# Kernel tuning notes

Hardware: AMD Instinct MI355X
Metric: run time of the kernel (lower is better)

## Reference

```python
import jax, jax.numpy as jnp
import numpy as np

N_NODES = 100000
BN_EPS = 1e-5


def gcn_conv(x, row, col, ew, W, b, n):
    # PyG GCNConv (normalize=True, add_self_loops=True):
    # add self loops with weight 1, symmetric deg^-1/2 normalization,
    # message = norm * (x @ W)[row], scatter-add at col (target), + bias.
    h = x @ W  # [N, F_out]
    loop = jnp.arange(n)
    row_f = jnp.concatenate([row, loop])
    col_f = jnp.concatenate([col, loop])
    ew_f = jnp.concatenate([ew, jnp.ones((n,), dtype=ew.dtype)])
    deg = jax.ops.segment_sum(ew_f, col_f, num_segments=n)  # [N]
    dis = jnp.where(deg > 0, jax.lax.rsqrt(jnp.maximum(deg, 1e-30)), 0.0)
    norm = dis[row_f] * ew_f * dis[col_f]  # [E+N]
    msg = norm[:, None] * h[row_f]  # [E+N, F_out]
    agg = jax.ops.segment_sum(msg, col_f, num_segments=n)
    return agg + b


def batchnorm(h, gamma, beta):
    mean = h.mean(axis=0)
    var = h.var(axis=0)  # biased, as torch BN training-mode normalization
    return gamma * (h - mean) * jax.lax.rsqrt(var + BN_EPS) + beta


def setup_inputs() -> dict:
    key = jax.random.key(0)
    ks = jax.random.split(key, 12)
    N, E, D = N_NODES, 3200000, 256
    x = jax.random.normal(ks[0], (N, D), dtype=jnp.float32)
    edge_index = jax.random.randint(ks[1], (2, E), 0, N, dtype=jnp.int64)
    edge_weight = jax.random.uniform(ks[2], (E,), dtype=jnp.float32)
    s = 1.0 / np.sqrt(D)
    W1 = jax.random.uniform(ks[3], (D, D), jnp.float32, -s, s)
    b1 = jnp.zeros((D,), jnp.float32)
    g1 = jnp.ones((D,), jnp.float32)
    be1 = jnp.zeros((D,), jnp.float32)
    W2 = jax.random.uniform(ks[4], (D, D), jnp.float32, -s, s)
    b2 = jnp.zeros((D,), jnp.float32)
    g2 = jnp.ones((D,), jnp.float32)
    be2 = jnp.zeros((D,), jnp.float32)
    return {"x": x, "edge_index": edge_index, "edge_weight": edge_weight,
            "W1": W1, "b1": b1, "g1": g1, "be1": be1,
            "W2": W2, "b2": b2, "g2": g2, "be2": be2}


def reference(x, edge_index, edge_weight, W1, b1, g1, be1, W2, b2, g2, be2):
    n = x.shape[0]
    row, col = edge_index[0], edge_index[1]
    h = gcn_conv(x, row, col, edge_weight, W1, b1, n)
    h = jax.nn.relu(batchnorm(h, g1, be1))
    h = gcn_conv(h, row, col, edge_weight, W2, b2, n)
    h = batchnorm(h, g2, be2)
    # in_dim == out_dim -> proj is Identity
    return jax.nn.relu(h + x)
```

## Files before the change

### kernel.cpp

```cpp
#include <hip/hip_runtime.h>
#include <hip/hip_bf16.h>

#define D 256
#define BN_EPS 1e-5f
#define CHUNK 4096
#define NPB 512
#define CAP_B 20480

typedef __attribute__((ext_vector_type(8))) short bf16x8;
typedef __attribute__((ext_vector_type(4))) float f32x4;
typedef unsigned long long ull;
typedef unsigned char uchar;

__device__ inline uint pack2_rne(float a, float b) {
    uint ua = __builtin_bit_cast(uint, a);
    ua = ua + 0x7FFFu + ((ua >> 16) & 1u);
    uint ub = __builtin_bit_cast(uint, b);
    ub = ub + 0x7FFFu + ((ub >> 16) & 1u);
    return (ua >> 16) | (ub & 0xFFFF0000u);
}
__device__ inline ushort f2bf_rne(float a) {
    uint ua = __builtin_bit_cast(uint, a);
    ua = ua + 0x7FFFu + ((ua >> 16) & 1u);
    return (ushort)(ua >> 16);
}
__device__ inline float bf2f(ushort u) {
    uint x = ((uint)u) << 16;
    return __builtin_bit_cast(float, x);
}
__device__ inline uint pack_edge(uint rowbits, uint ewbits) {
    uint b15 = (ewbits + 0x8000u) >> 16;
    return (rowbits & 0x1FFFFu) | (b15 << 17);
}
__device__ inline float edge_ew(uint e) {
    return __builtin_bit_cast(float, (e >> 17) << 16);
}

__global__ __launch_bounds__(256) void init_fast_kernel(int* __restrict__ cursor,
                                                        float* __restrict__ stats) {
    int t = threadIdx.x;
    cursor[t] = t * CAP_B;
    stats[t] = 0.f;
    stats[t + 256] = 0.f;
    stats[t + 512] = 0.f;
    stats[t + 768] = 0.f;
}

__global__ __launch_bounds__(256) void bin_kernel(const int* __restrict__ row,
                                                  const int* __restrict__ col,
                                                  const float* __restrict__ ew,
                                                  int* __restrict__ cursor,
                                                  uint2* __restrict__ bdata, int E) {
    __shared__ int h[256];
    __shared__ int base[256];
    int t = threadIdx.x;
    h[t] = 0;
    __syncthreads();
    int cb = blockIdx.x * CHUNK;
    int cols[CHUNK / 256];
#pragma unroll
    for (int i = 0; i < CHUNK / 256; ++i) {
        int e = cb + i * 256 + t;
        int c = (e < E) ? col[e] : -1;
        cols[i] = c;
        if (c >= 0) atomicAdd(&h[c >> 9], 1);
    }
    __syncthreads();
    if (h[t]) base[t] = atomicAdd(&cursor[t], h[t]);
    __syncthreads();
    h[t] = 0;
    __syncthreads();
#pragma unroll
    for (int i = 0; i < CHUNK / 256; ++i) {
        int e = cb + i * 256 + t;
        int c = cols[i];
        if (c >= 0) {
            int b = c >> 9;
            int pos = base[b] + atomicAdd(&h[b], 1);
            if (pos < (b + 1) * CAP_B) {
                uint xv = (uint)row[e] | ((uint)(c & (NPB - 1)) << 17);
                bdata[pos] = make_uint2(xv, __float_as_uint(ew[e]));
            }
        }
    }
}

__global__ __launch_bounds__(256) void final_csr_kernel(const uint2* __restrict__ bdata,
                                                        const int* __restrict__ cursor,
                                                        uint* __restrict__ csr,
                                                        int* __restrict__ offs,
                                                        int* __restrict__ cnts,
                                                        float2* __restrict__ dscale, int N) {
    __shared__ int cnt[NPB];
    __shared__ float deg[NPB];
    __shared__ int sp[256];
    int bkt = blockIdx.x;
    int t = threadIdx.x;
    int beg = bkt * CAP_B;
    int end = min(cursor[bkt], beg + CAP_B);
    cnt[t] = 0; cnt[t + 256] = 0;
    deg[t] = 0.f; deg[t + 256] = 0.f;
    __syncthreads();
    for (int i = beg + t; i < end; i += 256) {
        uint2 v = bdata[i];
        int cl = v.x >> 17;
        atomicAdd(&cnt[cl], 1);
        atomicAdd(&deg[cl], __uint_as_float(v.y));
    }
    __syncthreads();
    int a0 = cnt[2 * t], a1 = cnt[2 * t + 1];
    sp[t] = a0 + a1;
    __syncthreads();
    for (int o = 1; o < 256; o <<= 1) {
        int add = (t >= o) ? sp[t - o] : 0;
        __syncthreads();
        sp[t] += add;
        __syncthreads();
    }
    int ex = sp[t] - (a0 + a1);
    int n0 = bkt * NPB + 2 * t;
    if (n0 < N) {
        offs[n0] = beg + ex;
        cnts[n0] = a0;
        dscale[n0].x = rsqrtf(deg[2 * t] + 1.0f);
    }
    if (n0 + 1 < N) {
        offs[n0 + 1] = beg + ex + a0;
        cnts[n0 + 1] = a1;
        dscale[n0 + 1].x = rsqrtf(deg[2 * t + 1] + 1.0f);
    }
    __syncthreads();
    cnt[2 * t] = ex;
    cnt[2 * t + 1] = ex + a0;
    __syncthreads();
    for (int i = beg + t; i < end; i += 256) {
        uint2 v = bdata[i];
        int cl = v.x >> 17;
        int pos = beg + atomicAdd(&cnt[cl], 1);
        csr[pos] = pack_edge(v.x, v.y);
    }
}

__global__ __launch_bounds__(256) void count_deg_kernel(const int* __restrict__ col,
                                                        const float* __restrict__ ew,
                                                        ull* __restrict__ dg, int E) {
    int e = blockIdx.x * 256 + threadIdx.x;
    if (e < E) {
        int c = col[e];
        uint q = (uint)(ew[e] * 8388608.0f + 0.5f);
        atomicAdd(&dg[c], (1ull << 40) | (ull)q);
    }
}

__global__ __launch_bounds__(256) void dis_cnt_kernel(const ull* __restrict__ dg,
                                                      float2* __restrict__ dscale,
                                                      int* __restrict__ cnt,
                                                      int* __restrict__ cnts,
                                                      float* __restrict__ stats, int N) {
    int i = blockIdx.x * 256 + threadIdx.x;
    if (i < 1024) stats[i] = 0.0f;
    if (i < N) {
        ull g = dg[i];
        int c = (int)(g >> 40);
        cnt[i] = c;
        cnts[i] = c;
        float deg = (float)(g & ((1ull << 40) - 1)) * (1.0f / 8388608.0f);
        dscale[i].x = rsqrtf(deg + 1.0f);
    }
}

__global__ __launch_bounds__(256) void scan_reduce(const int* __restrict__ cnt,
                                                   int* __restrict__ bsum, int N) {
    __shared__ int sd[256];
    int t = threadIdx.x;
    int i = blockIdx.x * 256 + t;
    sd[t] = (i < N) ? cnt[i] : 0;
    __syncthreads();
    for (int o = 128; o > 0; o >>= 1) {
        if (t < o) sd[t] += sd[t + o];
        __syncthreads();
    }
    if (t == 0) bsum[blockIdx.x] = sd[0];
}

__global__ __launch_bounds__(512) void scan_bsum(int* __restrict__ bsum, int B) {
    __shared__ int sd[512];
    int t = threadIdx.x;
    int v = (t < B) ? bsum[t] : 0;
    sd[t] = v;
    __syncthreads();
    for (int o = 1; o < 512; o <<= 1) {
        int add = (t >= o) ? sd[t - o] : 0;
        __syncthreads();
        sd[t] += add;
        __syncthreads();
    }
    if (t < B) bsum[t] = sd[t] - v;
}

__global__ __launch_bounds__(256) void scan_final(const int* __restrict__ cnt,
                                                  const int* __restrict__ bsum,
                                                  int* __restrict__ offs,
                                                  int* __restrict__ next, int N, int E) {
    __shared__ int sd[256];
    int t = threadIdx.x;
    int i = blockIdx.x * 256 + t;
    int v = (i < N) ? cnt[i] : 0;
    sd[t] = v;
    __syncthreads();
    for (int o = 1; o < 256; o <<= 1) {
        int add = (t >= o) ? sd[t - o] : 0;
        __syncthreads();
        sd[t] += add;
        __syncthreads();
    }
    int excl = sd[t] - v + bsum[blockIdx.x];
    if (i < N) {
        offs[i] = excl;
        next[i] = excl;
    }
    if (i == 0 && blockIdx.x == 0) offs[N] = E;
}

__global__ __launch_bounds__(256) void fill_kernel(const int* __restrict__ row,
                                                   const int* __restrict__ col,
                                                   const float* __restrict__ ew,
                                                   int* __restrict__ next,
                                                   uint* __restrict__ csr, int E) {
    int e = blockIdx.x * 256 + threadIdx.x;
    if (e < E) {
        int pos = atomicAdd(&next[col[e]], 1);
        csr[pos] = pack_edge((uint)row[e], __float_as_uint(ew[e]));
    }
}

__global__ __launch_bounds__(256) void prep_wt2_kernel(const float* __restrict__ W1,
                                                       const float* __restrict__ W2,
                                                       ushort* __restrict__ Wt1,
                                                       ushort* __restrict__ Wt2) {
    __shared__ float tile[64][65];
    const float* W = blockIdx.y ? W2 : W1;
    ushort* Wt = blockIdx.y ? Wt2 : Wt1;
    int t = threadIdx.x;
    int k0 = (blockIdx.x >> 2) * 64;
    int n0 = (blockIdx.x & 3) * 64;
#pragma unroll
    for (int it = 0; it < 16; ++it) {
        int idx = it * 256 + t;
        int r = idx >> 6, c = idx & 63;
        tile[r][c] = W[(size_t)(k0 + r) * D + n0 + c];
    }
    __syncthreads();
#pragma unroll
    for (int it = 0; it < 16; ++it) {
        int idx = it * 256 + t;
        int n = idx >> 6, k = idx & 63;
        Wt[(size_t)(n0 + n) * D + k0 + k] = f2bf_rne(tile[k][n]);
    }
}

template <int MODE>
__global__ __launch_bounds__(256) void gemm_mfma(const float* __restrict__ Xf,
                                                 const ushort* __restrict__ Xb,
                                                 const float* __restrict__ stats,
                                                 const float* __restrict__ gamma,
                                                 const float* __restrict__ beta,
                                                 const ushort* __restrict__ Wt,
                                                 uchar* __restrict__ Hq,
                                                 float2* __restrict__ dscale,
                                                 int N, float invN) {
    __shared__ char wt_lds[32 * 1024];
    __shared__ float cf_lds[2][MODE ? 256 : 1];
    const int t = threadIdx.x;
    const int wv = t >> 6;
    const int l = t & 63;
    const int ln = l & 15;
    const int kg0 = l >> 4;
    const int rblk = blockIdx.x * 128 + wv * 32;

    if constexpr (MODE == 1) {
        float mean = stats[t] * invN;
        float var = fmaxf(stats[D + t] * invN - mean * mean, 0.0f);
        float sc = gamma[t] * rsqrtf(var + BN_EPS);
        cf_lds[0][t] = sc;
        cf_lds[1][t] = beta[t] - sc * mean;
    }

    f32x4 acc[2][16];
#pragma unroll
    for (int g = 0; g < 2; ++g)
#pragma unroll
        for (int i = 0; i < 16; ++i) acc[g][i] = f32x4{0.f, 0.f, 0.f, 0.f};

    const int sg_n = t >> 3;
    const int sg_g = t & 7;
    const int sg_lds = (sg_g ^ (sg_n & 7)) * 16;

    for (int kt = 0; kt < 4; ++kt) {
        const int k0 = kt * 64;
        __syncthreads();
#pragma unroll
        for (int p = 0; p < 8; ++p) {
            int n = p * 32 + sg_n;
            uint4 v = *reinterpret_cast<const uint4*>(Wt + (size_t)n * 256 + k0 + sg_g * 8);
            *reinterpret_cast<uint4*>(&wt_lds[n * 128 + sg_lds]) = v;
        }
        __syncthreads();
#pragma unroll
        for (int kh = 0; kh < 2; ++kh) {
            const int kb = k0 + kh * 32 + kg0 * 8;
            bf16x8 afr[2];
#pragma unroll
            for (int g = 0; g < 2; ++g) {
                int arow = rblk + g * 16 + ln;
                afr[g] = bf16x8{};
                if (arow < N) {
                    if constexpr (MODE == 0) {
                        const float* ap = Xf + (size_t)arow * D + kb;
                        float4 f0 = *reinterpret_cast<const float4*>(ap);
                        float4 f1 = *reinterpret_cast<const float4*>(ap + 4);
                        uint4 u;
                        u.x = (__builtin_bit_cast(uint, f0.x) >> 16) | (__builtin_bit_cast(uint, f0.y) & 0xFFFF0000u);
                        u.y = (__builtin_bit_cast(uint, f0.z) >> 16) | (__builtin_bit_cast(uint, f0.w) & 0xFFFF0000u);
                        u.z = (__builtin_bit_cast(uint, f1.x) >> 16) | (__builtin_bit_cast(uint, f1.y) & 0xFFFF0000u);
                        u.w = (__builtin_bit_cast(uint, f1.z) >> 16) | (__builtin_bit_cast(uint, f1.w) & 0xFFFF0000u);
                        afr[g] = __builtin_bit_cast(bf16x8, u);
                    } else {
                        bf16x8 raw = *reinterpret_cast<const bf16x8*>(Xb + (size_t)arow * D + kb);
                        f32x4 scA = *reinterpret_cast<const f32x4*>(&cf_lds[0][kb]);
                        f32x4 scB = *reinterpret_cast<const f32x4*>(&cf_lds[0][kb + 4]);
                        f32x4 shA = *reinterpret_cast<const f32x4*>(&cf_lds[1][kb]);
                        f32x4 shB = *reinterpret_cast<const f32x4*>(&cf_lds[1][kb + 4]);
                        uint4 u;
                        u.x = pack2_rne(fmaxf(scA[0] * bf2f((ushort)raw[0]) + shA[0], 0.f),
                                        fmaxf(scA[1] * bf2f((ushort)raw[1]) + shA[1], 0.f));
                        u.y = pack2_rne(fmaxf(scA[2] * bf2f((ushort)raw[2]) + shA[2], 0.f),
                                        fmaxf(scA[3] * bf2f((ushort)raw[3]) + shA[3], 0.f));
                        u.z = pack2_rne(fmaxf(scB[0] * bf2f((ushort)raw[4]) + shB[0], 0.f),
                                        fmaxf(scB[1] * bf2f((ushort)raw[5]) + shB[1], 0.f));
                        u.w = pack2_rne(fmaxf(scB[2] * bf2f((ushort)raw[6]) + shB[2], 0.f),
                                        fmaxf(scB[3] * bf2f((ushort)raw[7]) + shB[3], 0.f));
                        afr[g] = __builtin_bit_cast(bf16x8, u);
                    }
                }
            }
            const int s = ln * 128 + (((kg0 + kh * 4) ^ (ln & 7)) * 16);
            const char* bbase = &wt_lds[s];
#pragma unroll
            for (int ct = 0; ct < 16; ++ct) {
                bf16x8 bfr = *reinterpret_cast<const bf16x8*>(bbase + ct * 2048);
                acc[0][ct] = __builtin_amdgcn_mfma_f32_16x16x32_bf16(afr[0], bfr, acc[0][ct], 0, 0, 0);
                acc[1][ct] = __builtin_amdgcn_mfma_f32_16x16x32_bf16(afr[1], bfr, acc[1][ct], 0, 0, 0);
            }
        }
    }

    __syncthreads();
    uchar* qtile = (uchar*)wt_lds;
#pragma unroll
    for (int g = 0; g < 2; ++g) {
#pragma unroll
        for (int r = 0; r < 4; ++r) {
            float am = 0.f;
#pragma unroll
            for (int ct = 0; ct < 16; ++ct) am = fmaxf(am, fabsf(acc[g][ct][r]));
#pragma unroll
            for (int mk = 1; mk < 16; mk <<= 1) am = fmaxf(am, __shfl_xor(am, mk));
            float qs = am > 0.f ? 127.0f / am : 0.f;
            int rloc = wv * 32 + g * 16 + kg0 * 4 + r;
            int rowi = blockIdx.x * 128 + rloc;
            if (ln == 0 && rowi < N) dscale[rowi].y = am * (1.0f / 127.0f);
#pragma unroll
            for (int ct = 0; ct < 16; ++ct) {
                int q = (int)rintf(acc[g][ct][r] * qs) + 128;
                qtile[rloc * 256 + ct * 16 + ln] = (uchar)q;
            }
        }
    }
    __syncthreads();
    const uint4* qt4 = reinterpret_cast<const uint4*>(qtile);
#pragma unroll
    for (int k = 0; k < 8; ++k) {
        int j = k * 256 + t;
        int rowi = blockIdx.x * 128 + (j >> 4);
        if (rowi < N)
            *reinterpret_cast<uint4*>(Hq + (size_t)rowi * 256 + (j & 15) * 16) = qt4[j];
    }
}

__global__ __launch_bounds__(128) void gather_q_kernel(const uchar* __restrict__ hq,
                                                       ushort* __restrict__ ha,
                                                       const uint* __restrict__ csr,
                                                       const int* __restrict__ offs,
                                                       const int* __restrict__ cnts,
                                                       const float2* __restrict__ dscale,
                                                       int N) {
    int node = blockIdx.x;
    int t = threadIdx.x;
    int wv = t >> 6;
    int ln = t & 63;
    int beg = offs[node];
    int cnt = cnts[node];
    float2 dsn = dscale[node];
    float dc = dsn.x;

    float a0 = 0.f, a1 = 0.f, a2 = 0.f, a3 = 0.f, S = 0.f;
    if (wv == 0) {
        float ws = dc * dc * dsn.y;
        uint q0 = *reinterpret_cast<const uint*>(hq + (size_t)node * 256 + ln * 4);
        a0 = ws * (float)(q0 & 0xFF);
        a1 = ws * (float)((q0 >> 8) & 0xFF);
        a2 = ws * (float)((q0 >> 16) & 0xFF);
        a3 = ws * (float)(q0 >> 24);
        S = ws;
    }

    __shared__ int2 sc[128];

    for (int base = 0; base < cnt; base += 128) {
        int m = min(128, cnt - base);
        if (t < m) {
            uint v = __builtin_nontemporal_load(csr + beg + base + t);
            int r = (int)(v & 0x1FFFFu);
            float2 dsr = dscale[r];
            float w = edge_ew(v) * dsr.x * dc * dsr.y;
            sc[t] = make_int2(r, __float_as_int(w));
        }
        __syncthreads();
        int i = wv;
        for (; i + 16 <= m; i += 16) {
            float w[8];
            uint v[8];
#pragma unroll
            for (int j = 0; j < 8; ++j) {
                int2 e = sc[i + 2 * j];
                w[j] = __int_as_float(e.y);
                v[j] = *reinterpret_cast<const uint*>(hq + (size_t)e.x * 256 + ln * 4);
            }
#pragma unroll
            for (int j = 0; j < 8; ++j) {
                a0 = fmaf(w[j], (float)(v[j] & 0xFF), a0);
                a1 = fmaf(w[j], (float)((v[j] >> 8) & 0xFF), a1);
                a2 = fmaf(w[j], (float)((v[j] >> 16) & 0xFF), a2);
                a3 = fmaf(w[j], (float)(v[j] >> 24), a3);
                S += w[j];
            }
        }
        for (; i < m; i += 2) {
            int2 e = sc[i];
            float w = __int_as_float(e.y);
            uint v = *reinterpret_cast<const uint*>(hq + (size_t)e.x * 256 + ln * 4);
            a0 = fmaf(w, (float)(v & 0xFF), a0);
            a1 = fmaf(w, (float)((v >> 8) & 0xFF), a1);
            a2 = fmaf(w, (float)((v >> 16) & 0xFF), a2);
            a3 = fmaf(w, (float)(v >> 24), a3);
            S += w;
        }
        __syncthreads();
    }

    __shared__ float4 redA[64];
    __shared__ float redS[64];
    if (wv == 1) {
        redA[ln] = make_float4(a0, a1, a2, a3);
        redS[ln] = S;
    }
    __syncthreads();
    if (wv == 0) {
        float4 rb = redA[ln];
        float Sb = redS[ln];
        a0 += rb.x; a1 += rb.y; a2 += rb.z; a3 += rb.w;
        S += Sb;
        float f0 = a0 - 128.0f * S;
        float f1 = a1 - 128.0f * S;
        float f2 = a2 - 128.0f * S;
        float f3 = a3 - 128.0f * S;
        uint2 p;
        p.x = pack2_rne(f0, f1);
        p.y = pack2_rne(f2, f3);
        reinterpret_cast<uint2*>(ha + (size_t)node * D)[ln] = p;
    }
}

__global__ __launch_bounds__(256) void stats_bf16_kernel(const ushort* __restrict__ ha,
                                                         float* __restrict__ stats, int N) {
    __shared__ float ls[512];
    int t = threadIdx.x;
    int tq = t & 63;
    int tr = t >> 6;
    float s[4] = {0.f, 0.f, 0.f, 0.f};
    float q[4] = {0.f, 0.f, 0.f, 0.f};
    for (int i = blockIdx.x * 4 + tr; i < N; i += gridDim.x * 4) {
        uint2 u = *reinterpret_cast<const uint2*>(ha + (size_t)i * D + tq * 4);
        float v0 = bf2f((ushort)u.x), v1 = bf2f((ushort)(u.x >> 16));
        float v2 = bf2f((ushort)u.y), v3 = bf2f((ushort)(u.y >> 16));
        s[0] += v0; q[0] += v0 * v0;
        s[1] += v1; q[1] += v1 * v1;
        s[2] += v2; q[2] += v2 * v2;
        s[3] += v3; q[3] += v3 * v3;
    }
    ls[t] = 0.f; ls[t + 256] = 0.f;
    __syncthreads();
#pragma unroll
    for (int j = 0; j < 4; ++j) {
        int c = tq * 4 + j;
        atomicAdd(&ls[c], s[j]);
        atomicAdd(&ls[256 + c], q[j]);
    }
    __syncthreads();
    for (int i = t; i < 512; i += 256)
        unsafeAtomicAdd(&stats[i], ls[i]);
}

__global__ __launch_bounds__(256) void final_kernel(const ushort* __restrict__ ha,
                                                    const float* __restrict__ x,
                                                    const float* __restrict__ stats2,
                                                    const float* __restrict__ gamma,
                                                    const float* __restrict__ beta,
                                                    float* __restrict__ out,
                                                    int N, float invN) {
    __shared__ float cf[2][256];
    int t = threadIdx.x;
    {
        float mean = stats2[t] * invN;
        float var = fmaxf(stats2[D + t] * invN - mean * mean, 0.0f);
        float sc = gamma[t] * rsqrtf(var + BN_EPS);
        cf[0][t] = sc;
        cf[1][t] = beta[t] - sc * mean;
    }
    __syncthreads();
    size_t i = (size_t)blockIdx.x * 256 + t;
    size_t total = (size_t)N * (D / 4);
    if (i >= total) return;
    int c0 = (int)((i * 4) & (D - 1));
    uint2 h = reinterpret_cast<const uint2*>(ha)[i];
    f32x4 xv = *(reinterpret_cast<const f32x4*>(x) + i);
    f32x4 sc4 = *reinterpret_cast<const f32x4*>(&cf[0][c0]);
    f32x4 sh4 = *reinterpret_cast<const f32x4*>(&cf[1][c0]);
    f32x4 o;
    o[0] = fmaxf(sc4[0] * bf2f((ushort)h.x) + sh4[0] + xv[0], 0.0f);
    o[1] = fmaxf(sc4[1] * bf2f((ushort)(h.x >> 16)) + sh4[1] + xv[1], 0.0f);
    o[2] = fmaxf(sc4[2] * bf2f((ushort)h.y) + sh4[2] + xv[2], 0.0f);
    o[3] = fmaxf(sc4[3] * bf2f((ushort)(h.y >> 16)) + sh4[3] + xv[3], 0.0f);
    __builtin_nontemporal_store(o, reinterpret_cast<f32x4*>(out) + i);
}

extern "C" void kernel_launch(void* const* d_in, const int* in_sizes, int n_in,
                              void* d_out, int out_size, void* d_ws, size_t ws_size,
                              hipStream_t stream) {
    const float* x  = (const float*)d_in[0];
    const int* eidx = (const int*)d_in[1];
    const float* ew = (const float*)d_in[2];
    const float* W1 = (const float*)d_in[3];
    const float* g1  = (const float*)d_in[5];
    const float* be1 = (const float*)d_in[6];
    const float* W2  = (const float*)d_in[7];
    const float* g2  = (const float*)d_in[9];
    const float* be2 = (const float*)d_in[10];
    float* out = (float*)d_out;

    const int N = in_sizes[0] / D;
    const int E = in_sizes[2];
    const int* row = eidx;
    const int* col = eidx + E;
    const float invN = 1.0f / (float)N;

    uchar* hq    = (uchar*)d_ws;
    ushort* ha   = (ushort*)(hq + (size_t)N * 256);
    ushort* Wt1  = ha + (size_t)N * D;
    ushort* Wt2  = Wt1 + 65536;
    float* stats = (float*)(Wt2 + 65536);
    float2* dscale = (float2*)(stats + 1024);
    int*   offs  = (int*)(dscale + N);
    int*   cnts  = offs + (N + 1);

    size_t head = (size_t)N * 256 + (size_t)N * D * 2 + (size_t)65536 * 4 + 1024 * 4
                + (size_t)N * 8 + (size_t)(N + 1) * 4 + (size_t)N * 4;

    const int nb = (N + NPB - 1) / NPB;
    const int nchunk = (E + CHUNK - 1) / CHUNK;
    const int scanB = (N + 255) / 256;
    const int gemmB = (N + 127) / 128;
    const int gElems4 = (N * (D / 4) + 255) / 256;

    size_t need_fast = head + 256 * 4 + 16 + (size_t)nb * CAP_B * 12;
    const bool fast = (N < (1 << 17)) && (nb <= 256) && (ws_size >= need_fast)
                   && ((size_t)nb * CAP_B >= (size_t)E);

    uint* csr;

    if (fast) {
        int* cursor = cnts + N;
        uintptr_t p = ((uintptr_t)(cursor + 256) + 15) & ~(uintptr_t)15;
        uint2* bdata = (uint2*)p;
        csr = (uint*)(bdata + (size_t)nb * CAP_B);

        init_fast_kernel<<<1, 256, 0, stream>>>(cursor, stats);
        bin_kernel<<<nchunk, 256, 0, stream>>>(row, col, ew, cursor, bdata, E);
        final_csr_kernel<<<nb, 256, 0, stream>>>(bdata, cursor, csr, offs, cnts, dscale, N);
    } else {
        int* cntnext = cnts + N;
        ull* dg   = (ull*)(cntnext + N);
        int* bsum = (int*)dg;
        csr = (uint*)(dg + N);
        hipMemsetAsync(dg, 0, (size_t)N * 8, stream);
        count_deg_kernel<<<(E + 255) / 256, 256, 0, stream>>>(col, ew, dg, E);
        dis_cnt_kernel<<<scanB, 256, 0, stream>>>(dg, dscale, cntnext, cnts, stats, N);
        scan_reduce<<<scanB, 256, 0, stream>>>(cntnext, bsum, N);
        scan_bsum<<<1, 512, 0, stream>>>(bsum, scanB);
        scan_final<<<scanB, 256, 0, stream>>>(cntnext, bsum, offs, cntnext, N, E);
        fill_kernel<<<(E + 255) / 256, 256, 0, stream>>>(row, col, ew, cntnext, csr, E);
    }

    prep_wt2_kernel<<<dim3(16, 2), 256, 0, stream>>>(W1, W2, Wt1, Wt2);

    gemm_mfma<0><<<gemmB, 256, 0, stream>>>(x, nullptr, nullptr, nullptr, nullptr,
                                            Wt1, hq, dscale, N, invN);
    gather_q_kernel<<<N, 128, 0, stream>>>(hq, ha, csr, offs, cnts, dscale, N);
    stats_bf16_kernel<<<1024, 256, 0, stream>>>(ha, stats, N);

    gemm_mfma<1><<<gemmB, 256, 0, stream>>>(nullptr, ha, stats, g1, be1,
                                            Wt2, hq, dscale, N, invN);
    gather_q_kernel<<<N, 128, 0, stream>>>(hq, ha, csr, offs, cnts, dscale, N);
    stats_bf16_kernel<<<1024, 256, 0, stream>>>(ha, stats + 512, N);

    final_kernel<<<gElems4, 256, 0, stream>>>(ha, x, stats + 512, g2, be2, out, N, invN);
}
```

Baseline: 627.5 us.

## Gather with one wavefront per node using 16-byte loads and shuffles

Measured after the change: 599.0 us. -4.5%, faster.

```diff
diff --git a/kernel.cpp b/kernel.cpp
--- a/kernel.cpp
+++ b/kernel.cpp
@@ -388,97 +388,79 @@
     }
 }
 
-__global__ __launch_bounds__(128) void gather_q_kernel(const uchar* __restrict__ hq,
+__global__ __launch_bounds__(256) void gather_q_kernel(const uchar* __restrict__ hq,
                                                        ushort* __restrict__ ha,
                                                        const uint* __restrict__ csr,
                                                        const int* __restrict__ offs,
                                                        const int* __restrict__ cnts,
                                                        const float2* __restrict__ dscale,
                                                        int N) {
-    int node = blockIdx.x;
-    int t = threadIdx.x;
-    int wv = t >> 6;
-    int ln = t & 63;
+    int wv = threadIdx.x >> 6;
+    int lane = threadIdx.x & 63;
+    int node = blockIdx.x * 4 + wv;
+    if (node >= N) return;
     int beg = offs[node];
     int cnt = cnts[node];
     float2 dsn = dscale[node];
     float dc = dsn.x;
-
-    float a0 = 0.f, a1 = 0.f, a2 = 0.f, a3 = 0.f, S = 0.f;
-    if (wv == 0) {
-        float ws = dc * dc * dsn.y;
-        uint q0 = *reinterpret_cast<const uint*>(hq + (size_t)node * 256 + ln * 4);
-        a0 = ws * (float)(q0 & 0xFF);
-        a1 = ws * (float)((q0 >> 8) & 0xFF);
-        a2 = ws * (float)((q0 >> 16) & 0xFF);
-        a3 = ws * (float)(q0 >> 24);
-        S = ws;
-    }
-
-    __shared__ int2 sc[128];
-
-    for (int base = 0; base < cnt; base += 128) {
-        int m = min(128, cnt - base);
-        if (t < m) {
-            uint v = __builtin_nontemporal_load(csr + beg + base + t);
-            int r = (int)(v & 0x1FFFFu);
+    int g = lane >> 4;
+    int u = lane & 15;
+
+    float acc[16];
+#pragma unroll
+    for (int j = 0; j < 16; ++j) acc[j] = 0.f;
+    float S = 0.f;
+
+    int total = cnt + 1;
+    for (int base = 0; base < total; base += 64) {
+        int m = min(64, total - base);
+        int gi = base + lane;
+        int r = node;
+        float w = 0.f;
+        if (gi < cnt) {
+            uint v = __builtin_nontemporal_load(csr + beg + gi);
+            r = (int)(v & 0x1FFFFu);
             float2 dsr = dscale[r];
-            float w = edge_ew(v) * dsr.x * dc * dsr.y;
-            sc[t] = make_int2(r, __float_as_int(w));
+            w = edge_ew(v) * dsr.x * dc * dsr.y;
+        } else if (gi == cnt) {
+            w = dc * dc * dsn.y;
         }
-        __syncthreads();
-        int i = wv;
-        for (; i + 16 <= m; i += 16) {
-            float w[8];
-            uint v[8];
-#pragma unroll
-            for (int j = 0; j < 8; ++j) {
-                int2 e = sc[i + 2 * j];
-                w[j] = __int_as_float(e.y);
-                v[j] = *reinterpret_cast<const uint*>(hq + (size_t)e.x * 256 + ln * 4);
-            }
-#pragma unroll
-            for (int j = 0; j < 8; ++j) {
-                a0 = fmaf(w[j], (float)(v[j] & 0xFF), a0);
-                a1 = fmaf(w[j], (float)((v[j] >> 8) & 0xFF), a1);
-                a2 = fmaf(w[j], (float)((v[j] >> 16) & 0xFF), a2);
-                a3 = fmaf(w[j], (float)(v[j] >> 24), a3);
-                S += w[j];
+        S += w;
+        for (int i = 0; i < m; i += 4) {
+            int src = i + g;
+            int er = __shfl(r, src);
+            float we = __shfl(w, src);
+            uint4 q = *reinterpret_cast<const uint4*>(hq + (size_t)er * 256 + u * 16);
+#pragma unroll
+            for (int b = 0; b < 4; ++b) {
+                uint qq = (&q.x)[b];
+                acc[b * 4 + 0] = fmaf(we, (float)(qq & 0xFF), acc[b * 4 + 0]);
+                acc[b * 4 + 1] = fmaf(we, (float)((qq >> 8) & 0xFF), acc[b * 4 + 1]);
+                acc[b * 4 + 2] = fmaf(we, (float)((qq >> 16) & 0xFF), acc[b * 4 + 2]);
+                acc[b * 4 + 3] = fmaf(we, (float)(qq >> 24), acc[b * 4 + 3]);
             }
         }
-        for (; i < m; i += 2) {
-            int2 e = sc[i];
-            float w = __int_as_float(e.y);
-            uint v = *reinterpret_cast<const uint*>(hq + (size_t)e.x * 256 + ln * 4);
-            a0 = fmaf(w, (float)(v & 0xFF), a0);
-            a1 = fmaf(w, (float)((v >> 8) & 0xFF), a1);
-            a2 = fmaf(w, (float)((v >> 16) & 0xFF), a2);
-            a3 = fmaf(w, (float)(v >> 24), a3);
-            S += w;
-        }
-        __syncthreads();
-    }
-
-    __shared__ float4 redA[64];
-    __shared__ float redS[64];
-    if (wv == 1) {
-        redA[ln] = make_float4(a0, a1, a2, a3);
-        redS[ln] = S;
-    }
-    __syncthreads();
-    if (wv == 0) {
-        float4 rb = redA[ln];
-        float Sb = redS[ln];
-        a0 += rb.x; a1 += rb.y; a2 += rb.z; a3 += rb.w;
-        S += Sb;
-        float f0 = a0 - 128.0f * S;
-        float f1 = a1 - 128.0f * S;
-        float f2 = a2 - 128.0f * S;
-        float f3 = a3 - 128.0f * S;
-        uint2 p;
-        p.x = pack2_rne(f0, f1);
-        p.y = pack2_rne(f2, f3);
-        reinterpret_cast<uint2*>(ha + (size_t)node * D)[ln] = p;
+    }
+
+#pragma unroll
+    for (int j = 0; j < 16; ++j) {
+        float a = acc[j];
+        a += __shfl_xor(a, 16);
+        a += __shfl_xor(a, 32);
+        acc[j] = a;
+    }
+#pragma unroll
+    for (int mk = 1; mk < 64; mk <<= 1) S += __shfl_xor(S, mk);
+
+    if (g == 0) {
+        float c = 128.0f * S;
+        uint o[8];
+#pragma unroll
+        for (int j = 0; j < 8; ++j)
+            o[j] = pack2_rne(acc[2 * j] - c, acc[2 * j + 1] - c);
+        uint4* dst = reinterpret_cast<uint4*>(ha + (size_t)node * D + u * 16);
+        dst[0] = make_uint4(o[0], o[1], o[2], o[3]);
+        dst[1] = make_uint4(o[4], o[5], o[6], o[7]);
     }
 }
 
@@ -614,14 +596,16 @@
 
     prep_wt2_kernel<<<dim3(16, 2), 256, 0, stream>>>(W1, W2, Wt1, Wt2);
 
+    const int gatherB = (N + 3) / 4;
+
     gemm_mfma<0><<<gemmB, 256, 0, stream>>>(x, nullptr, nullptr, nullptr, nullptr,
                                             Wt1, hq, dscale, N, invN);
-    gather_q_kernel<<<N, 128, 0, stream>>>(hq, ha, csr, offs, cnts, dscale, N);
+    gather_q_kernel<<<gatherB, 256, 0, stream>>>(hq, ha, csr, offs, cnts, dscale, N);
     stats_bf16_kernel<<<1024, 256, 0, stream>>>(ha, stats, N);
 
     gemm_mfma<1><<<gemmB, 256, 0, stream>>>(nullptr, ha, stats, g1, be1,
                                             Wt2, hq, dscale, N, invN);
-    gather_q_kernel<<<N, 128, 0, stream>>>(hq, ha, csr, offs, cnts, dscale, N);
+    gather_q_kernel<<<gatherB, 256, 0, stream>>>(hq, ha, csr, offs, cnts, dscale, N);
     stats_bf16_kernel<<<1024, 256, 0, stream>>>(ha, stats + 512, N);
 
     final_kernel<<<gElems4, 256, 0, stream>>>(ha, x, stats + 512, g2, be2, out, N, invN);
```
